# Optimization experiments

Hardware: AMD Instinct MI355X
Metric: run time of the kernel (lower is better)

Reference implementation:

```python
import jax, jax.numpy as jnp
import numpy as np

B, S, D = 2, 2048, 1024
N_HEADS, D_HEAD = 16, 64
INIT_STD = 0.02


def setup_inputs() -> dict:
    key = jax.random.key(0)
    k_res, k_q, k_k, k_v, k_o = jax.random.split(key, 5)
    residual = jax.random.normal(k_res, (B, S, D), dtype=jnp.float32)
    W_Q = INIT_STD * jax.random.normal(k_q, (N_HEADS, D_HEAD, D), dtype=jnp.float32)
    W_K = INIT_STD * jax.random.normal(k_k, (N_HEADS, D_HEAD, D), dtype=jnp.float32)
    W_V = INIT_STD * jax.random.normal(k_v, (N_HEADS, D_HEAD, D), dtype=jnp.float32)
    W_O = INIT_STD * jax.random.normal(k_o, (N_HEADS, D_HEAD, D), dtype=jnp.float32)
    return {"residual": residual, "W_Q": W_Q, "W_K": W_K, "W_V": W_V, "W_O": W_O}


def reference(residual, W_Q, W_K, W_V, W_O):
    seq_len = residual.shape[1]
    # projections: [b, n, p, h]  (heads first, matching q.transpose(1,2))
    q = jnp.einsum('bpd,nhd->bnph', residual, W_Q)
    k = jnp.einsum('bpd,nhd->bnph', residual, W_K)
    v = jnp.einsum('bpd,nhd->bnph', residual, W_V)
    scale = 1.0 / jnp.sqrt(jnp.asarray(q.shape[-1], dtype=residual.dtype))
    # [b, n, p_q, p_k] full score matrix (faithful to original naive impl)
    scores = jnp.einsum('bnqh,bnkh->bnqk', q, k) * scale
    causal = jnp.tril(jnp.ones((seq_len, seq_len), dtype=bool))
    scores = jnp.where(causal, scores, -jnp.inf)
    pattern = jax.nn.softmax(scores, axis=-1)
    attn_out = jnp.einsum('bnqk,bnkh->bnqh', pattern, v)
    # output projection summed over heads: 'bpnh,nhd->bpd'
    return jnp.einsum('bnph,nhd->bpd', attn_out, W_O)
```

## Files before the change

### kernel.cpp

```cpp
#include <hip/hip_runtime.h>
#include <math.h>


#define SS_ 2048
#define DD_ 1024
#define NH_ 16
#define BN_ 32
#define BS_ 4096

typedef __bf16 bf16x8 __attribute__((ext_vector_type(8)));
typedef __bf16 bf16x4 __attribute__((ext_vector_type(4)));
typedef short shortx4 __attribute__((ext_vector_type(4)));
typedef float floatx4 __attribute__((ext_vector_type(4)));
typedef unsigned short ushortx4 __attribute__((ext_vector_type(4)));

__device__ __forceinline__ unsigned short f2bf(float f) {
    union { float f; unsigned u; } v; v.f = f;
    unsigned r = v.u + 0x7FFFu + ((v.u >> 16) & 1u);
    return (unsigned short)(r >> 16);
}

__device__ __forceinline__ floatx4 mfma_pv(bf16x4 a, bf16x4 b, floatx4 c) {
#if __has_builtin(__builtin_amdgcn_mfma_f32_16x16x16_bf16)
    return __builtin_amdgcn_mfma_f32_16x16x16_bf16(a, b, c, 0, 0, 0);
#else
    return __builtin_amdgcn_mfma_f32_16x16x16bf16_1k(
        __builtin_bit_cast(shortx4, a), __builtin_bit_cast(shortx4, b), c, 0, 0, 0);
#endif
}

__device__ __forceinline__ void gl_lds16(const unsigned short* g, unsigned short* l) {
    __builtin_amdgcn_global_load_lds(
        (const __attribute__((address_space(1))) unsigned int*)g,
        (__attribute__((address_space(3))) unsigned int*)l, 16, 0, 0);
}

__global__ __launch_bounds__(256) void cast_bf16_kernel(
    const float* __restrict__ resid, const float* __restrict__ WQ,
    const float* __restrict__ WK, const float* __restrict__ WV,
    unsigned short* __restrict__ residB, unsigned short* __restrict__ WQb,
    unsigned short* __restrict__ WKb, unsigned short* __restrict__ WVb)
{
    const int x = blockIdx.x;
    int z, ix;
    if (x < 4096) { z = 0; ix = x; }
    else { z = 1 + ((x - 4096) >> 10); ix = (x - 4096) & 1023; }
    const float* src = (z == 0) ? resid : (z == 1) ? WQ : (z == 2) ? WK : WV;
    unsigned short* dst = (z == 0) ? residB : (z == 1) ? WQb : (z == 2) ? WKb : WVb;
    const int i = (ix * 256 + threadIdx.x) * 4;
    float4 f = *(const float4*)(src + i);
    ushortx4 o;
    o[0] = f2bf(f.x); o[1] = f2bf(f.y); o[2] = f2bf(f.z); o[3] = f2bf(f.w);
    *(ushortx4*)(dst + i) = o;
}

__global__ __launch_bounds__(256) void wo_transpose_kernel(
    const float* __restrict__ WO, unsigned short* __restrict__ WOt)
{
    __shared__ float t[64][65];
    const int kk0 = blockIdx.x * 64, d0 = blockIdx.y * 64;
    #pragma unroll
    for (int it = 0; it < 16; ++it) {
        int idx = it * 256 + threadIdx.x;
        int r = idx >> 6, c = idx & 63;
        t[r][c] = WO[(kk0 + r) * DD_ + d0 + c];
    }
    __syncthreads();
    #pragma unroll
    for (int it = 0; it < 16; ++it) {
        int idx = it * 256 + threadIdx.x;
        int r = idx >> 6, c = idx & 63;
        WOt[(d0 + r) * DD_ + kk0 + c] = f2bf(t[c][r]);
    }
}

__global__ __launch_bounds__(256) void qkv_m97_kernel(
    const unsigned short* __restrict__ residB,
    const unsigned short* __restrict__ WQb,
    const unsigned short* __restrict__ WKb,
    const unsigned short* __restrict__ WVb,
    unsigned short* __restrict__ q, unsigned short* __restrict__ kk,
    unsigned short* __restrict__ vT)
{
    __shared__ unsigned short As[64 * 64];
    __shared__ unsigned short Bs[128 * 64];
    const int tid = threadIdx.x;
    const int l = tid & 63, w = tid >> 6;
    const int quad = l >> 4, lan = l & 15;
    const int z = blockIdx.z;
    const unsigned short* W = (z == 0) ? WQb : (z == 1) ? WKb : WVb;
    unsigned short* dst = (z == 0) ? q : (z == 1) ? kk : vT;
    const int mBase = blockIdx.x * 64;
    const int nBase = blockIdx.y * 128;
    const int wm = (w & 1) * 32, wn = (w >> 1) * 64;

    floatx4 acc[2][4];
    #pragma unroll
    for (int a = 0; a < 2; ++a)
        #pragma unroll
        for (int b = 0; b < 4; ++b)
            #pragma unroll
            for (int i = 0; i < 4; ++i) acc[a][b][i] = 0.f;

    const int sr = l >> 3;
    const int sgx = ((l & 7) ^ sr) * 8;

    for (int k0 = 0; k0 < DD_; k0 += 64) {
        __syncthreads();
        #pragma unroll
        for (int i = 0; i < 2; ++i) {
            const int row = i * 32 + w * 8 + sr;
            gl_lds16(residB + (size_t)(mBase + row) * DD_ + k0 + sgx,
                     As + i * 2048 + w * 512);
        }
        #pragma unroll
        for (int i = 0; i < 4; ++i) {
            const int row = i * 32 + w * 8 + sr;
            gl_lds16(W + (size_t)(nBase + row) * DD_ + k0 + sgx,
                     Bs + i * 2048 + w * 512);
        }
        __syncthreads();
        #pragma unroll
        for (int ks = 0; ks < 2; ++ks) {
            const int fo = (((ks * 4 + quad) ^ (lan & 7)) << 3);
            bf16x8 a[2], b[4];
            #pragma unroll
            for (int mi = 0; mi < 2; ++mi)
                a[mi] = *(const bf16x8*)(As + (wm + mi * 16 + lan) * 64 + fo);
            #pragma unroll
            for (int ni = 0; ni < 4; ++ni)
                b[ni] = *(const bf16x8*)(Bs + (wn + ni * 16 + lan) * 64 + fo);
            #pragma unroll
            for (int mi = 0; mi < 2; ++mi)
                #pragma unroll
                for (int ni = 0; ni < 4; ++ni)
                    acc[mi][ni] = __builtin_amdgcn_mfma_f32_16x16x32_bf16(
                        a[mi], b[ni], acc[mi][ni], 0, 0, 0);
        }
    }
    const int headU = (nBase + wn) >> 6;
    if (z == 1) {
        #pragma unroll
        for (int mi = 0; mi < 2; ++mi)
            #pragma unroll
            for (int ni = 0; ni < 4; ++ni)
                #pragma unroll
                for (int reg = 0; reg < 4; ++reg) {
                    int m = mBase + wm + mi * 16 + quad * 4 + reg;
                    int bb = m >> 11, ss = m & 2047;
                    int h = ni * 16 + lan;
                    dst[((size_t)(bb * NH_ + headU) * SS_ + ss) * 64 + h] =
                        f2bf(acc[mi][ni][reg]);
                }
    } else {
        const float scl = (z == 0) ? 0.125f * 1.44269504088896340736f : 1.0f;
        #pragma unroll
        for (int mi = 0; mi < 2; ++mi) {
            const int m0 = mBase + wm + mi * 16 + quad * 4;
            const int bb = m0 >> 11, ss0 = m0 & 2047;
            #pragma unroll
            for (int ni = 0; ni < 4; ++ni) {
                const int h = ni * 16 + lan;
                bf16x4 ob;
                #pragma unroll
                for (int reg = 0; reg < 4; ++reg)
                    ob[reg] = static_cast<__bf16>(acc[mi][ni][reg] * scl);
                *(bf16x4*)(dst + ((size_t)(bb * NH_ + headU) * 64 + h) * SS_ + ss0) = ob;
            }
        }
    }
}

__global__ __launch_bounds__(256, 4) void flash_mfma_kernel(
    const unsigned short* __restrict__ q,
    const unsigned short* __restrict__ k,
    const unsigned short* __restrict__ vT,
    unsigned short* __restrict__ attn)
{
    __shared__ unsigned short ldsK[3][64 * 64];
    __shared__ unsigned short ldsV[2][64 * 64];
    const int l = threadIdx.x & 63, w = threadIdx.x >> 6;
    const int quad = l >> 4, lan = l & 15;
    const int f = blockIdx.x;
    const int bn = (f & 7) | (((f >> 3) & 3) << 3);
    const int g = f >> 5;
    const int ch = (g < 8) ? (31 - g)
                 : (g < 16) ? (g + 8)
                 : (g < 24) ? (15 - (g - 16))
                 : (g - 24);

    const unsigned short* Qg = q  + (size_t)bn * 64 * SS_;
    const unsigned short* Kg = k  + (size_t)bn * SS_ * 64;
    const unsigned short* Vg = vT + (size_t)bn * 64 * SS_;

    const int srl = l >> 3;
    const int sgx = (l & 7) ^ srl;

    const int qRow0 = ch * 64 + w * 16;
    const int qAbs = qRow0 + lan;

    bf16x8 Qf0, Qf1;
    #pragma unroll
    for (int j = 0; j < 8; ++j) {
        Qf0[j] = *(const __bf16*)(Qg + (size_t)(quad * 8 + j) * SS_ + qAbs);
        Qf1[j] = *(const __bf16*)(Qg + (size_t)(quad * 8 + j + 32) * SS_ + qAbs);
    }

    bf16x4 ones;
    #pragma unroll
    for (int i = 0; i < 4; ++i) ones[i] = static_cast<__bf16>(1.0f);

    float mrow = -INFINITY;
    floatx4 l_acc;
    floatx4 o[4];
    #pragma unroll
    for (int i = 0; i < 4; ++i) l_acc[i] = 0.f;
    #pragma unroll
    for (int t = 0; t < 4; ++t)
        #pragma unroll
        for (int i = 0; i < 4; ++i) o[t][i] = 0.f;

    #define STAGE_K(kt_, buf_)                                                  \
        { const int row0_ = w * 16, kB_ = (kt_) * 64;                           \
          gl_lds16(Kg + (size_t)(kB_ + row0_ + srl) * 64 + sgx * 8,             \
                   &ldsK[buf_][row0_ * 64]);                                    \
          gl_lds16(Kg + (size_t)(kB_ + row0_ + 8 + srl) * 64 + sgx * 8,         \
                   &ldsK[buf_][(row0_ + 8) * 64]); }
    #define STAGE_V(kt_, buf_)                                                  \
        { const int row0_ = w * 16, kB_ = (kt_) * 64;                           \
          gl_lds16(Vg + (size_t)(row0_ + srl) * SS_ + kB_ + sgx * 8,            \
                   &ldsV[buf_][row0_ * 64]);                                    \
          gl_lds16(Vg + (size_t)(row0_ + 8 + srl) * SS_ + kB_ + sgx * 8,        \
                   &ldsV[buf_][(row0_ + 8) * 64]); }
    #define QK_TILE(dst_, buf_)                                                 \
        { const unsigned short* Kb_ = &ldsK[buf_][0];                           \
          bf16x8 K0v_[4], K1v_[4];                                              \
          _Pragma("unroll")                                                     \
          for (int nt = 0; nt < 4; ++nt) {                                      \
              const unsigned short* kr_ = Kb_ + (nt * 16 + lan) * 64;           \
              K0v_[nt] = *(const bf16x8*)(kr_ + ((quad ^ (lan & 7)) << 3));     \
              K1v_[nt] = *(const bf16x8*)(kr_ + (((quad + 4) ^ (lan & 7)) << 3)); } \
          _Pragma("unroll")                                                     \
          for (int nt = 0; nt < 4; ++nt) {                                      \
              floatx4 zz_; zz_[0] = zz_[1] = zz_[2] = zz_[3] = 0.f;             \
              dst_[nt] = __builtin_amdgcn_mfma_f32_16x16x32_bf16(K0v_[nt], Qf0, zz_, 0, 0, 0); \
              dst_[nt] = __builtin_amdgcn_mfma_f32_16x16x32_bf16(K1v_[nt], Qf1, dst_[nt], 0, 0, 0); } }

    STAGE_K(0, 0);
    STAGE_V(0, 0);
    __syncthreads();
    if (ch >= 1) STAGE_K(1, 1);
    floatx4 scCur[4], scNext[4];
    QK_TILE(scCur, 0);

    for (int kt = 0; kt <= ch; ++kt) {
        const int kBase = kt * 64;
        __syncthreads();
        if (kt + 2 <= ch) STAGE_K(kt + 2, (kt + 2) % 3);
        if (kt + 1 <= ch) {
            STAGE_V(kt + 1, (kt + 1) & 1);
            QK_TILE(scNext, (kt + 1) % 3);
        }
        const unsigned short* Vb = &ldsV[kt & 1][0];
        bf16x4 Vfv[4][4];
        #pragma unroll
        for (int t = 0; t < 4; ++t) {
            const unsigned short* vr = Vb + (t * 16 + lan) * 64 + ((quad & 1) << 2);
            #pragma unroll
            for (int nt = 0; nt < 4; ++nt) {
                const int g2 = nt * 2 + (quad >> 1);
                Vfv[t][nt] = *(const bf16x4*)(vr + ((g2 ^ (lan & 7)) << 3));
            }
        }
        if (kt == ch) {
            #pragma unroll
            for (int nt = 0; nt < 4; ++nt)
                #pragma unroll
                for (int reg = 0; reg < 4; ++reg)
                    if (kBase + nt * 16 + quad * 4 + reg > qAbs)
                        scCur[nt][reg] = -INFINITY;
        }
        float mx = scCur[0][0];
        #pragma unroll
        for (int nt = 0; nt < 4; ++nt)
            #pragma unroll
            for (int reg = 0; reg < 4; ++reg) mx = fmaxf(mx, scCur[nt][reg]);
        mx = fmaxf(mx, __shfl_xor(mx, 16, 64));
        mx = fmaxf(mx, __shfl_xor(mx, 32, 64));
        const float mnew = fmaxf(mrow, mx);
        if (!__all(mx <= mrow)) {
            const float alpha = exp2f(mrow - mnew);
            l_acc[0] *= alpha;
            #pragma unroll
            for (int t = 0; t < 4; ++t)
                #pragma unroll
                for (int i = 0; i < 4; ++i) o[t][i] *= alpha;
        }
        mrow = mnew;
        bf16x4 pb[4];
        #pragma unroll
        for (int nt = 0; nt < 4; ++nt)
            #pragma unroll
            for (int reg = 0; reg < 4; ++reg)
                pb[nt][reg] = static_cast<__bf16>(exp2f(scCur[nt][reg] - mnew));
        #pragma unroll
        for (int nt = 0; nt < 4; ++nt)
            l_acc = mfma_pv(ones, pb[nt], l_acc);
        #pragma unroll
        for (int t = 0; t < 4; ++t)
            #pragma unroll
            for (int nt = 0; nt < 4; ++nt)
                o[t] = mfma_pv(Vfv[t][nt], pb[nt], o[t]);
        #pragma unroll
        for (int nt = 0; nt < 4; ++nt) scCur[nt] = scNext[nt];
    }
    const float rl = 1.f / l_acc[0];
    #pragma unroll
    for (int t = 0; t < 4; ++t) {
        bf16x4 ob;
        #pragma unroll
        for (int reg = 0; reg < 4; ++reg)
            ob[reg] = static_cast<__bf16>(o[t][reg] * rl);
        *(bf16x4*)(attn + ((size_t)bn * SS_ + qAbs) * 64 + t * 16 + quad * 4) = ob;
    }
    #undef STAGE_K
    #undef STAGE_V
    #undef QK_TILE
}

__global__ __launch_bounds__(256) void out_m97_kernel(
    const unsigned short* __restrict__ attn,
    const unsigned short* __restrict__ WOt,
    float* __restrict__ out)
{
    __shared__ unsigned short As[64 * 64];
    __shared__ unsigned short Bs[128 * 64];
    const int tid = threadIdx.x;
    const int l = tid & 63, w = tid >> 6;
    const int quad = l >> 4, lan = l & 15;
    const int mBase = blockIdx.x * 64;
    const int nBase = blockIdx.y * 128;
    const int wm = (w & 1) * 32, wn = (w >> 1) * 64;
    const int bbU = mBase >> 11;
    const int ssBase = mBase & 2047;

    floatx4 acc[2][4];
    #pragma unroll
    for (int a = 0; a < 2; ++a)
        #pragma unroll
        for (int b = 0; b < 4; ++b)
            #pragma unroll
            for (int i = 0; i < 4; ++i) acc[a][b][i] = 0.f;

    const int sr = l >> 3;
    const int sgx = ((l & 7) ^ sr) * 8;

    for (int kt = 0; kt < 16; ++kt) {
        const int k0 = kt * 64;
        __syncthreads();
        #pragma unroll
        for (int i = 0; i < 2; ++i) {
            const int row = i * 32 + w * 8 + sr;
            gl_lds16(attn + ((size_t)(bbU * NH_ + kt) * SS_ + ssBase + row) * 64 + sgx,
                     As + i * 2048 + w * 512);
        }
        #pragma unroll
        for (int i = 0; i < 4; ++i) {
            const int row = i * 32 + w * 8 + sr;
            gl_lds16(WOt + (size_t)(nBase + row) * DD_ + k0 + sgx,
                     Bs + i * 2048 + w * 512);
        }
        __syncthreads();
        #pragma unroll
        for (int ks = 0; ks < 2; ++ks) {
            const int fo = (((ks * 4 + quad) ^ (lan & 7)) << 3);
            bf16x8 a[2], b[4];
            #pragma unroll
            for (int mi = 0; mi < 2; ++mi)
                a[mi] = *(const bf16x8*)(As + (wm + mi * 16 + lan) * 64 + fo);
            #pragma unroll
            for (int ni = 0; ni < 4; ++ni)
                b[ni] = *(const bf16x8*)(Bs + (wn + ni * 16 + lan) * 64 + fo);
            #pragma unroll
            for (int mi = 0; mi < 2; ++mi)
                #pragma unroll
                for (int ni = 0; ni < 4; ++ni)
                    acc[mi][ni] = __builtin_amdgcn_mfma_f32_16x16x32_bf16(
                        a[mi], b[ni], acc[mi][ni], 0, 0, 0);
        }
    }
    #pragma unroll
    for (int mi = 0; mi < 2; ++mi)
        #pragma unroll
        for (int ni = 0; ni < 4; ++ni)
            #pragma unroll
            for (int reg = 0; reg < 4; ++reg) {
                int m = mBase + wm + mi * 16 + quad * 4 + reg;
                out[(size_t)m * DD_ + nBase + wn + ni * 16 + lan] = acc[mi][ni][reg];
            }
}

extern "C" void kernel_launch(void* const* d_in, const int* in_sizes, int n_in,
                              void* d_out, int out_size, void* d_ws, size_t ws_size,
                              hipStream_t stream) {
    const float* resid = (const float*)d_in[0];
    const float* WQ    = (const float*)d_in[1];
    const float* WK    = (const float*)d_in[2];
    const float* WV    = (const float*)d_in[3];
    const float* WO    = (const float*)d_in[4];
    float* out = (float*)d_out;

    unsigned short* q      = (unsigned short*)d_ws;
    unsigned short* kk     = q      + 4194304;
    unsigned short* vT     = kk     + 4194304;
    unsigned short* attn   = vT     + 4194304;
    unsigned short* residB = attn   + 4194304;
    unsigned short* WQb    = residB + 4194304;
    unsigned short* WKb    = WQb    + 1048576;
    unsigned short* WVb    = WKb    + 1048576;
    unsigned short* WOt    = WVb    + 1048576;

    cast_bf16_kernel<<<dim3(7168), 256, 0, stream>>>(
        resid, WQ, WK, WV, residB, WQb, WKb, WVb);
    wo_transpose_kernel<<<dim3(16, 16), 256, 0, stream>>>(WO, WOt);
    qkv_m97_kernel<<<dim3(64, 8, 3), 256, 0, stream>>>(
        residB, WQb, WKb, WVb, q, kk, vT);
    flash_mfma_kernel<<<dim3(1024), dim3(256), 0, stream>>>(q, kk, vT, attn);
    out_m97_kernel<<<dim3(64, 8), 256, 0, stream>>>(attn, WOt, out);
}
```

Baseline: 180.6 us.

## Fuse Q, K, V projections into one kernel sharing the residual tile

Replaces the three-way z-dimension QKV GEMM launch with one kernel per (128-row, head) tile. Each tile loads the residual slab once into LDS and multiplies it against the Q, K and V weight slices for that head. This cuts repeated residual loads and puts 512 threads with 12 accumulators per wave in each block. In exchange each wave does only 16 rows, so the A fragment is reused less per load, and the grid drops to 512 blocks from 1536.

```diff
diff --git a/kernel.cpp b/kernel.cpp
--- a/kernel.cpp
+++ b/kernel.cpp
@@ -74,7 +74,7 @@
     }
 }
 
-__global__ __launch_bounds__(256) void qkv_m97_kernel(
+__global__ __launch_bounds__(512, 4) void qkv_fused_kernel(
     const unsigned short* __restrict__ residB,
     const unsigned short* __restrict__ WQb,
     const unsigned short* __restrict__ WKb,
@@ -82,92 +82,78 @@
     unsigned short* __restrict__ q, unsigned short* __restrict__ kk,
     unsigned short* __restrict__ vT)
 {
-    __shared__ unsigned short As[64 * 64];
-    __shared__ unsigned short Bs[128 * 64];
+    __shared__ unsigned short As[128 * 64];
+    __shared__ unsigned short Bq[64 * 64];
+    __shared__ unsigned short Bk[64 * 64];
+    __shared__ unsigned short Bv[64 * 64];
     const int tid = threadIdx.x;
     const int l = tid & 63, w = tid >> 6;
     const int quad = l >> 4, lan = l & 15;
-    const int z = blockIdx.z;
-    const unsigned short* W = (z == 0) ? WQb : (z == 1) ? WKb : WVb;
-    unsigned short* dst = (z == 0) ? q : (z == 1) ? kk : vT;
-    const int mBase = blockIdx.x * 64;
-    const int nBase = blockIdx.y * 128;
-    const int wm = (w & 1) * 32, wn = (w >> 1) * 64;
-
-    floatx4 acc[2][4];
-    #pragma unroll
-    for (int a = 0; a < 2; ++a)
-        #pragma unroll
-        for (int b = 0; b < 4; ++b)
-            #pragma unroll
-            for (int i = 0; i < 4; ++i) acc[a][b][i] = 0.f;
+    const int mBase = blockIdx.x * 128;
+    const int head = blockIdx.y;
+    const int nBase = head * 64;
+
+    floatx4 accQ[4], accK[4], accV[4];
+    #pragma unroll
+    for (int ni = 0; ni < 4; ++ni)
+        #pragma unroll
+        for (int i = 0; i < 4; ++i) {
+            accQ[ni][i] = 0.f; accK[ni][i] = 0.f; accV[ni][i] = 0.f;
+        }
 
     const int sr = l >> 3;
     const int sgx = ((l & 7) ^ sr) * 8;
 
     for (int k0 = 0; k0 < DD_; k0 += 64) {
         __syncthreads();
-        #pragma unroll
-        for (int i = 0; i < 2; ++i) {
-            const int row = i * 32 + w * 8 + sr;
-            gl_lds16(residB + (size_t)(mBase + row) * DD_ + k0 + sgx,
-                     As + i * 2048 + w * 512);
-        }
-        #pragma unroll
-        for (int i = 0; i < 4; ++i) {
-            const int row = i * 32 + w * 8 + sr;
-            gl_lds16(W + (size_t)(nBase + row) * DD_ + k0 + sgx,
-                     Bs + i * 2048 + w * 512);
-        }
+        gl_lds16(residB + (size_t)(mBase + w * 16 + sr) * DD_ + k0 + sgx,
+                 As + (w * 16) * 64);
+        gl_lds16(residB + (size_t)(mBase + w * 16 + 8 + sr) * DD_ + k0 + sgx,
+                 As + (w * 16 + 8) * 64);
+        gl_lds16(WQb + (size_t)(nBase + w * 8 + sr) * DD_ + k0 + sgx,
+                 Bq + (w * 8) * 64);
+        gl_lds16(WKb + (size_t)(nBase + w * 8 + sr) * DD_ + k0 + sgx,
+                 Bk + (w * 8) * 64);
+        gl_lds16(WVb + (size_t)(nBase + w * 8 + sr) * DD_ + k0 + sgx,
+                 Bv + (w * 8) * 64);
         __syncthreads();
         #pragma unroll
         for (int ks = 0; ks < 2; ++ks) {
             const int fo = (((ks * 4 + quad) ^ (lan & 7)) << 3);
-            bf16x8 a[2], b[4];
-            #pragma unroll
-            for (int mi = 0; mi < 2; ++mi)
-                a[mi] = *(const bf16x8*)(As + (wm + mi * 16 + lan) * 64 + fo);
-            #pragma unroll
-            for (int ni = 0; ni < 4; ++ni)
-                b[ni] = *(const bf16x8*)(Bs + (wn + ni * 16 + lan) * 64 + fo);
-            #pragma unroll
-            for (int mi = 0; mi < 2; ++mi)
-                #pragma unroll
-                for (int ni = 0; ni < 4; ++ni)
-                    acc[mi][ni] = __builtin_amdgcn_mfma_f32_16x16x32_bf16(
-                        a[mi], b[ni], acc[mi][ni], 0, 0, 0);
-        }
-    }
-    const int headU = (nBase + wn) >> 6;
-    if (z == 1) {
-        #pragma unroll
-        for (int mi = 0; mi < 2; ++mi)
-            #pragma unroll
-            for (int ni = 0; ni < 4; ++ni)
-                #pragma unroll
-                for (int reg = 0; reg < 4; ++reg) {
-                    int m = mBase + wm + mi * 16 + quad * 4 + reg;
-                    int bb = m >> 11, ss = m & 2047;
-                    int h = ni * 16 + lan;
-                    dst[((size_t)(bb * NH_ + headU) * SS_ + ss) * 64 + h] =
-                        f2bf(acc[mi][ni][reg]);
-                }
-    } else {
-        const float scl = (z == 0) ? 0.125f * 1.44269504088896340736f : 1.0f;
-        #pragma unroll
-        for (int mi = 0; mi < 2; ++mi) {
-            const int m0 = mBase + wm + mi * 16 + quad * 4;
-            const int bb = m0 >> 11, ss0 = m0 & 2047;
+            bf16x8 a = *(const bf16x8*)(As + (w * 16 + lan) * 64 + fo);
+            bf16x8 bq[4], bk[4], bv[4];
             #pragma unroll
             for (int ni = 0; ni < 4; ++ni) {
-                const int h = ni * 16 + lan;
-                bf16x4 ob;
-                #pragma unroll
-                for (int reg = 0; reg < 4; ++reg)
-                    ob[reg] = static_cast<__bf16>(acc[mi][ni][reg] * scl);
-                *(bf16x4*)(dst + ((size_t)(bb * NH_ + headU) * 64 + h) * SS_ + ss0) = ob;
+                bq[ni] = *(const bf16x8*)(Bq + (ni * 16 + lan) * 64 + fo);
+                bk[ni] = *(const bf16x8*)(Bk + (ni * 16 + lan) * 64 + fo);
+                bv[ni] = *(const bf16x8*)(Bv + (ni * 16 + lan) * 64 + fo);
             }
-        }
+            #pragma unroll
+            for (int ni = 0; ni < 4; ++ni) {
+                accQ[ni] = __builtin_amdgcn_mfma_f32_16x16x32_bf16(a, bq[ni], accQ[ni], 0, 0, 0);
+                accK[ni] = __builtin_amdgcn_mfma_f32_16x16x32_bf16(a, bk[ni], accK[ni], 0, 0, 0);
+                accV[ni] = __builtin_amdgcn_mfma_f32_16x16x32_bf16(a, bv[ni], accV[ni], 0, 0, 0);
+            }
+        }
+    }
+    const int m0 = mBase + w * 16 + quad * 4;
+    const int bb = m0 >> 11, ss0 = m0 & 2047;
+    const float scl = 0.125f * 1.44269504088896340736f;
+    #pragma unroll
+    for (int ni = 0; ni < 4; ++ni) {
+        const int h = ni * 16 + lan;
+        bf16x4 obq, obv;
+        #pragma unroll
+        for (int reg = 0; reg < 4; ++reg) {
+            obq[reg] = static_cast<__bf16>(accQ[ni][reg] * scl);
+            obv[reg] = static_cast<__bf16>(accV[ni][reg]);
+        }
+        *(bf16x4*)(q  + ((size_t)(bb * NH_ + head) * 64 + h) * SS_ + ss0) = obq;
+        *(bf16x4*)(vT + ((size_t)(bb * NH_ + head) * 64 + h) * SS_ + ss0) = obv;
+        #pragma unroll
+        for (int reg = 0; reg < 4; ++reg)
+            kk[((size_t)(bb * NH_ + head) * SS_ + ss0 + reg) * 64 + h] =
+                f2bf(accK[ni][reg]);
     }
 }
 
@@ -423,7 +409,7 @@
     cast_bf16_kernel<<<dim3(7168), 256, 0, stream>>>(
         resid, WQ, WK, WV, residB, WQb, WKb, WVb);
     wo_transpose_kernel<<<dim3(16, 16), 256, 0, stream>>>(WO, WOt);
-    qkv_m97_kernel<<<dim3(64, 8, 3), 256, 0, stream>>>(
+    qkv_fused_kernel<<<dim3(32, 16), 512, 0, stream>>>(
         residB, WQb, WKb, WVb, q, kk, vT);
     flash_mfma_kernel<<<dim3(1024), dim3(256), 0, stream>>>(q, kk, vT, attn);
     out_m97_kernel<<<dim3(64, 8), 256, 0, stream>>>(attn, WOt, out);
```

New measurement: 174.9 us. 3.1% less time.
